# Kernel optimization log

Measured on AMD Instinct MI355X. Metric: run time of the kernel, lower is better.

## Reference

```python
import jax, jax.numpy as jnp
import numpy as np

NE, NPROC, E, D = 50000, 25000, 200000, 128
L, T = 3, 4  # layers, edge types: 0:e->e, 1:e->p, 2:p->p, 3:p->e


def setup_inputs() -> dict:
    key = jax.random.key(0)
    ks = jax.random.split(key, 17)
    s = 1.0 / np.sqrt(D)
    return {
        'x_elem': jax.random.normal(ks[0], (NE, D), jnp.float32),
        'x_proc': jax.random.normal(ks[1], (NPROC, D), jnp.float32),
        'W_src': jax.random.normal(ks[2], (L, T, D, D), jnp.float32) * s,
        'W_dst': jax.random.normal(ks[3], (L, T, D, D), jnp.float32) * s,
        'att_src': jax.random.normal(ks[4], (L, T, D), jnp.float32) * s,
        'att_dst': jax.random.normal(ks[5], (L, T, D), jnp.float32) * s,
        'bias': jax.random.normal(ks[6], (L, T, D), jnp.float32) * 0.01,
        'lin_W': jax.random.normal(ks[7], (D, 2), jnp.float32) * s,
        'lin_b': jnp.zeros((2,), jnp.float32),
        'ee_src': jax.random.randint(ks[8], (E,), 0, NE),
        'ee_dst': jax.random.randint(ks[9], (E,), 0, NE),
        'ep_src': jax.random.randint(ks[10], (E,), 0, NE),
        'ep_dst': jax.random.randint(ks[11], (E,), 0, NPROC),
        'pp_src': jax.random.randint(ks[12], (E,), 0, NPROC),
        'pp_dst': jax.random.randint(ks[13], (E,), 0, NPROC),
        'pe_src': jax.random.randint(ks[14], (E,), 0, NPROC),
        'pe_dst': jax.random.randint(ks[15], (E,), 0, NE),
    }


def _gat(x_s, x_d, src, dst, n_dst, Ws, Wd, a_s, a_d, b):
    # one GATConv (heads=1, negative_slope=0 -> relu, no self loops)
    hs = x_s @ Ws                       # [Ns, D]
    hd = x_d @ Wd                       # [Nd, D]
    es = hs @ a_s                       # [Ns]
    ed = hd @ a_d                       # [Nd]
    logit = jax.nn.relu(es[src] + ed[dst])              # [E]
    m = jax.ops.segment_max(logit, dst, num_segments=n_dst)
    m = jnp.where(jnp.isfinite(m), m, 0.0)              # empty segments
    w = jnp.exp(logit - m[dst])
    denom = jax.ops.segment_sum(w, dst, num_segments=n_dst)
    alpha = w / jnp.maximum(denom[dst], 1e-16)          # edge softmax per dst
    out = jax.ops.segment_sum(alpha[:, None] * hs[src], dst, num_segments=n_dst)
    return out + b


def reference(x_elem, x_proc, W_src, W_dst, att_src, att_dst, bias, lin_W, lin_b,
              ee_src, ee_dst, ep_src, ep_dst, pp_src, pp_dst, pe_src, pe_dst):
    xe, xp = x_elem, x_proc
    for l in range(L):
        ee = _gat(xe, xe, ee_src, ee_dst, NE, W_src[l, 0], W_dst[l, 0], att_src[l, 0], att_dst[l, 0], bias[l, 0])
        ep = _gat(xe, xp, ep_src, ep_dst, NPROC, W_src[l, 1], W_dst[l, 1], att_src[l, 1], att_dst[l, 1], bias[l, 1])
        pp = _gat(xp, xp, pp_src, pp_dst, NPROC, W_src[l, 2], W_dst[l, 2], att_src[l, 2], att_dst[l, 2], bias[l, 2])
        pe = _gat(xp, xe, pe_src, pe_dst, NE, W_src[l, 3], W_dst[l, 3], att_src[l, 3], att_dst[l, 3], bias[l, 3])
        xe = ee + pe   # to_hetero aggr='sum' per destination node type
        xp = ep + pp
    x = jnp.concatenate([xe, xp], axis=0) @ lin_W + lin_b  # G_aggr
    return x.mean(axis=0)  # [2]
```

## Files before the change

kernel.cpp:

```cpp
#include <hip/hip_runtime.h>

#define NE_N 50000
#define NP_N 25000
#define E_N 200000
#define DIM 128
#define LOG2E 1.4426950408889634f
#define NREP 1024

#define NCHK 32
#define CHK_E (E_N / NCHK)
#define TBL 16384

typedef __attribute__((ext_vector_type(8))) short short8;
typedef __attribute__((ext_vector_type(4))) float f32x4;
typedef __attribute__((ext_vector_type(2))) float f32x2;

static __device__ __forceinline__ ushort f2bf(float f) {
  unsigned x = __float_as_uint(f);
  return (ushort)((x + 0x7fffu + ((x >> 16) & 1u)) >> 16);
}
static __device__ __forceinline__ float bf2f(ushort u) {
  return __uint_as_float(((unsigned)u) << 16);
}

static __device__ __forceinline__ void gload_lds16(const void* g, void* l) {
  __builtin_amdgcn_global_load_lds(
      (const __attribute__((address_space(1))) void*)g,
      (__attribute__((address_space(3))) void*)l, 16, 0, 0);
}

#define HIST_BLKS (4 * NCHK)
#define HS_TOT (HIST_BLKS + 12 + 3)
__global__ __launch_bounds__(512) void hist_setup_k(
    const float* __restrict__ W_src, const float* __restrict__ W_dst,
    const float* __restrict__ att_dst, ushort* __restrict__ WbT,
    float* __restrict__ vec, const int* __restrict__ d0,
    const int* __restrict__ d1, const int* __restrict__ d2,
    const int* __restrict__ d3, unsigned char* __restrict__ h0,
    unsigned char* __restrict__ h1, unsigned char* __restrict__ h2,
    unsigned char* __restrict__ h3, ushort* __restrict__ rk0,
    ushort* __restrict__ rk1, ushort* __restrict__ rk2,
    ushort* __restrict__ rk3) {
  __shared__ int keys[TBL];
  __shared__ int cnts[TBL];
  const int blk = blockIdx.x;
  const int tid = threadIdx.x;
  if (blk < HIST_BLKS) {
    const int ty = blk >> 5, c = blk & (NCHK - 1);
    const int NN = (ty == 0 || ty == 3) ? NE_N : NP_N;
    const int* dst = ty == 0 ? d0 : ty == 1 ? d1 : ty == 2 ? d2 : d3;
    unsigned char* h = ty == 0 ? h0 : ty == 1 ? h1 : ty == 2 ? h2 : h3;
    ushort* rk = ty == 0 ? rk0 : ty == 1 ? rk1 : ty == 2 ? rk2 : rk3;
    for (int i = tid; i < TBL; i += 512) { keys[i] = -1; cnts[i] = 0; }
    __syncthreads();
    const int base = c * CHK_E;
    for (int i = tid; i < CHK_E; i += 512) {
      const int e = base + i;
      const int d = dst[e];
      unsigned hsh = ((unsigned)d * 2654435761u) >> 18;
      hsh &= (TBL - 1);
      int lr;
      while (true) {
        int prev = atomicCAS(&keys[hsh], -1, d);
        if (prev == -1 || prev == d) { lr = atomicAdd(&cnts[hsh], 1); break; }
        hsh = (hsh + 1) & (TBL - 1);
      }
      rk[e] = (ushort)lr;
    }
    __syncthreads();
    for (int i = tid; i < TBL; i += 512) {
      int k = keys[i];
      if (k >= 0) h[(size_t)c * NN + k] = (unsigned char)cnts[i];
    }
  } else if (blk < HIST_BLKS + 12) {
    const int w = blk - HIST_BLKS;
    const float* src = W_src + (size_t)w * DIM * DIM;
    ushort* dstw = WbT + (size_t)w * DIM * DIM;
    for (int i = tid; i < DIM * DIM; i += 512) {
      int k = i >> 7, n = i & 127;
      dstw[n * DIM + k] = f2bf(src[i]);
    }
  } else {
    const int b = blk - HIST_BLKS - 12;
    const int lt = b * 4 + (tid >> 7);
    const int i = tid & 127;
    const float* Wd = W_dst + (size_t)lt * DIM * DIM;
    const float* ad = att_dst + lt * DIM;
    float s = 0.f;
#pragma unroll 8
    for (int j = 0; j < DIM; j++) s += Wd[i * DIM + j] * ad[j];
    vec[lt * DIM + i] = s;
  }
}

__global__ __launch_bounds__(256) void scanA_k(
    unsigned char* __restrict__ h0, unsigned char* __restrict__ h1,
    unsigned char* __restrict__ h2, unsigned char* __restrict__ h3,
    int* __restrict__ c0, int* __restrict__ c1, int* __restrict__ c2,
    int* __restrict__ c3, int* __restrict__ part) {
  int ty = blockIdx.y;
  unsigned char* h = ty == 0 ? h0 : ty == 1 ? h1 : ty == 2 ? h2 : h3;
  int* cnt = ty == 0 ? c0 : ty == 1 ? c1 : ty == 2 ? c2 : c3;
  int n = (ty == 0 || ty == 3) ? NE_N : NP_N;
  int nblk = (n + 1023) >> 10;
  if ((int)blockIdx.x >= nblk) return;
  int base = blockIdx.x * 1024 + threadIdx.x * 4;
  int s = 0;
  if (base < n) {
    int run0 = 0, run1 = 0, run2 = 0, run3 = 0;
#pragma unroll
    for (int c = 0; c < NCHK; c++) {
      unsigned* hp = (unsigned*)(h + (size_t)c * n + base);
      unsigned v = *hp;
      *hp = (unsigned)(run0 & 255) | ((unsigned)(run1 & 255) << 8) |
            ((unsigned)(run2 & 255) << 16) | ((unsigned)(run3 & 255) << 24);
      run0 += (int)(v & 255u);
      run1 += (int)((v >> 8) & 255u);
      run2 += (int)((v >> 16) & 255u);
      run3 += (int)((v >> 24) & 255u);
    }
    cnt[base + 0] = run0; cnt[base + 1] = run1;
    cnt[base + 2] = run2; cnt[base + 3] = run3;
    s = run0 + run1 + run2 + run3;
  }
  int lane = threadIdx.x & 63, wid = threadIdx.x >> 6;
#pragma unroll
  for (int off = 32; off > 0; off >>= 1) s += __shfl_xor(s, off, 64);
  __shared__ int ws4[4];
  if (lane == 0) ws4[wid] = s;
  __syncthreads();
  if (threadIdx.x == 0)
    part[ty * 64 + blockIdx.x] = ws4[0] + ws4[1] + ws4[2] + ws4[3];
}

__global__ __launch_bounds__(256) void scanBC_k(
    const int* __restrict__ c0, const int* __restrict__ c1,
    const int* __restrict__ c2, const int* __restrict__ c3,
    int* __restrict__ r0, int* __restrict__ r1, int* __restrict__ r2,
    int* __restrict__ r3, const int* __restrict__ part) {
  int ty = blockIdx.y;
  int bx = blockIdx.x;
  const int* cnt = ty == 0 ? c0 : ty == 1 ? c1 : ty == 2 ? c2 : c3;
  int* rp = ty == 0 ? r0 : ty == 1 ? r1 : ty == 2 ? r2 : r3;
  int n = (ty == 0 || ty == 3) ? NE_N : NP_N;
  int nblk = (n + 1023) >> 10;
  if (bx >= nblk) return;

  __shared__ int s_excl;
  if (threadIdx.x < 64) {
    int pl = threadIdx.x;
    int v = (pl < nblk) ? part[ty * 64 + pl] : 0;
    int sc = v;
#pragma unroll
    for (int off = 1; off < 64; off <<= 1) {
      int t = __shfl_up(sc, off, 64);
      if (pl >= off) sc += t;
    }
    if (pl == bx) s_excl = sc - v;
  }
  if (bx == 0 && threadIdx.x == 0) rp[n] = E_N;
  __syncthreads();

  int base = bx * 1024 + threadIdx.x * 4;
  int v[4];
#pragma unroll
  for (int j = 0; j < 4; j++) v[j] = (base + j < n) ? cnt[base + j] : 0;
  int s = v[0] + v[1] + v[2] + v[3];
  int lane = threadIdx.x & 63, wid = threadIdx.x >> 6;
  int sc = s;
#pragma unroll
  for (int off = 1; off < 64; off <<= 1) {
    int t = __shfl_up(sc, off, 64);
    if (lane >= off) sc += t;
  }
  __shared__ int ws4[4];
  if (lane == 63) ws4[wid] = sc;
  __syncthreads();
  int wbase = 0;
  for (int w = 0; w < wid; w++) wbase += ws4[w];
  int p = s_excl + wbase + sc - s;
#pragma unroll
  for (int j = 0; j < 4; j++) {
    if (base + j < n) rp[base + j] = p;
    p += v[j];
  }
}

#define EBLK ((NE_N + 255) / 256)
#define PBLK ((NP_N + 255) / 256)
#define GEMM_BLK (EBLK + PBLK)
#define FILL_PER_CHK 13
#define FILL_BLKS (4 * NCHK * FILL_PER_CHK)
#define HG2_TOT (GEMM_BLK + FILL_BLKS)

template <bool FP32>
static __device__ __forceinline__ void x_prefetch(
    const void* xb, int rowA, int quad, float4* xraw, short8* xvv) {
  if (FP32) {
    const float* xf32 = (const float*)xb + (size_t)rowA * DIM + quad * 8;
#pragma unroll
    for (int k0 = 0; k0 < 4; k0++) {
      xraw[2 * k0] = *(const float4*)(xf32 + k0 * 32);
      xraw[2 * k0 + 1] = *(const float4*)(xf32 + k0 * 32 + 4);
    }
  } else {
    const ushort* xb16 = (const ushort*)xb + (size_t)rowA * DIM + quad * 8;
#pragma unroll
    for (int k0 = 0; k0 < 4; k0++)
      xvv[k0] = *(const short8*)(xb16 + k0 * 32);
  }
}

template <bool FP32>
static __device__ __forceinline__ void strip_body(
    int row0, int N, int m, int quad, int lane, const short8* wlds,
    const float* dv0, const float* dv1, const float* a0, const float* a1,
    unsigned char* hs0, unsigned char* hs1, float* es0, float* es1,
    float* edA, float* edB, float4* xraw, short8* xvv) {
  float edp0 = 0.f, edp1 = 0.f;
#pragma unroll
  for (int k0 = 0; k0 < 4; k0++) {
    float xf[8];
    if (FP32) {
      float4 f0 = xraw[2 * k0], f1 = xraw[2 * k0 + 1];
      xf[0] = f0.x; xf[1] = f0.y; xf[2] = f0.z; xf[3] = f0.w;
      xf[4] = f1.x; xf[5] = f1.y; xf[6] = f1.z; xf[7] = f1.w;
      short8 xv;
#pragma unroll
      for (int j = 0; j < 8; j++) xv[j] = (short)f2bf(xf[j]);
      xvv[k0] = xv;
    } else {
#pragma unroll
      for (int j = 0; j < 8; j++) xf[j] = bf2f((ushort)xvv[k0][j]);
    }
    int off = k0 * 32 + quad * 8;
    float4 vA0 = *(const float4*)&dv0[off];
    float4 vA1 = *(const float4*)&dv0[off + 4];
    float4 vB0 = *(const float4*)&dv1[off];
    float4 vB1 = *(const float4*)&dv1[off + 4];
    edp0 += xf[0] * vA0.x + xf[1] * vA0.y + xf[2] * vA0.z + xf[3] * vA0.w +
            xf[4] * vA1.x + xf[5] * vA1.y + xf[6] * vA1.z + xf[7] * vA1.w;
    edp1 += xf[0] * vB0.x + xf[1] * vB0.y + xf[2] * vB0.z + xf[3] * vB0.w +
            xf[4] * vB1.x + xf[5] * vB1.y + xf[6] * vB1.z + xf[7] * vB1.w;
  }

  f32x4 acc0[8], acc1[8];
#pragma unroll
  for (int f = 0; f < 8; f++) {
    acc0[f] = (f32x4){0.f, 0.f, 0.f, 0.f};
    acc1[f] = (f32x4){0.f, 0.f, 0.f, 0.f};
  }
#pragma unroll
  for (int k0 = 0; k0 < 4; k0++) {
    const short8 xv = xvv[k0];
#pragma unroll
    for (int f = 0; f < 8; f++) {
      acc0[f] = __builtin_amdgcn_mfma_f32_16x16x32_bf16(
          wlds[(k0 * 8 + f) * 64 + lane], xv, acc0[f], 0, 0, 0);
      acc1[f] = __builtin_amdgcn_mfma_f32_16x16x32_bf16(
          wlds[2048 + (k0 * 8 + f) * 64 + lane], xv, acc1[f], 0, 0, 0);
    }
  }

  const int row = row0 + m;
  edp0 += __shfl_xor(edp0, 16, 64);
  edp0 += __shfl_xor(edp0, 32, 64);
  edp1 += __shfl_xor(edp1, 16, 64);
  edp1 += __shfl_xor(edp1, 32, 64);
  if (quad == 0 && row < N) {
    edA[row] = edp0 * LOG2E;
    edB[row] = edp1 * LOG2E;
  }

#pragma unroll
  for (int set = 0; set < 2; set++) {
    f32x4* acc = set ? acc1 : acc0;
    const float* as = set ? a1 : a0;
    float* es = set ? es1 : es0;
    unsigned char* hs = set ? hs1 : hs0;

    float esum = 0.f;
#pragma unroll
    for (int f = 0; f < 8; f++) {
      float4 av = *(const float4*)&as[f * 16 + quad * 4];
      esum += acc[f][0] * av.x + acc[f][1] * av.y + acc[f][2] * av.z +
              acc[f][3] * av.w;
    }
    esum += __shfl_xor(esum, 16, 64);
    esum += __shfl_xor(esum, 32, 64);
    if (quad == 0 && row < N) es[row] = esum * LOG2E;

    if (row < N) {
#pragma unroll
      for (int f = 0; f < 8; f++) {
        int w = __builtin_amdgcn_cvt_pk_fp8_f32(acc[f][0], acc[f][1], 0, false);
        w = __builtin_amdgcn_cvt_pk_fp8_f32(acc[f][2], acc[f][3], w, true);
        *(unsigned*)&hs[(size_t)row * DIM + f * 16 + quad * 4] = (unsigned)w;
      }
    }
  }
}

template <bool FP32>
static __device__ __forceinline__ void gemm_body(
    int blk, const void* __restrict__ xev, const void* __restrict__ xpv,
    const ushort* __restrict__ WbT, const float* __restrict__ att,
    const float* __restrict__ vec, int l, unsigned char* __restrict__ hsE0,
    unsigned char* __restrict__ hsE1, unsigned char* __restrict__ hsP3,
    unsigned char* __restrict__ hsP2, float* __restrict__ esE0,
    float* __restrict__ esE1, float* __restrict__ esP3,
    float* __restrict__ esP2, float* __restrict__ edEA,
    float* __restrict__ edEB, float* __restrict__ edPA,
    float* __restrict__ edPB) {
  const void* xb;
  const ushort *W0T, *W1T;
  const float *a0, *a1, *dv0, *dv1;
  unsigned char *hs0, *hs1;
  float *es0, *es1, *edA, *edB;
  int N, rbase;
  if (blk < EBLK) {
    xb = xev; N = NE_N; rbase = blk * 256;
    W0T = WbT + (size_t)(l * 4 + 0) * DIM * DIM;
    W1T = WbT + (size_t)(l * 4 + 1) * DIM * DIM;
    a0 = att + (l * 4 + 0) * DIM; a1 = att + (l * 4 + 1) * DIM;
    dv0 = vec + (l * 4 + 0) * DIM; dv1 = vec + (l * 4 + 3) * DIM;
    hs0 = hsE0; hs1 = hsE1; es0 = esE0; es1 = esE1;
    edA = edEA; edB = edEB;
  } else {
    blk -= EBLK; xb = xpv; N = NP_N; rbase = blk * 256;
    W0T = WbT + (size_t)(l * 4 + 3) * DIM * DIM;
    W1T = WbT + (size_t)(l * 4 + 2) * DIM * DIM;
    a0 = att + (l * 4 + 3) * DIM; a1 = att + (l * 4 + 2) * DIM;
    dv0 = vec + (l * 4 + 1) * DIM; dv1 = vec + (l * 4 + 2) * DIM;
    hs0 = hsP3; hs1 = hsP2; es0 = esP3; es1 = esP2;
    edA = edPA; edB = edPB;
  }

  const int wave = threadIdx.x >> 6;
  const int lane = threadIdx.x & 63;
  const int m = lane & 15, quad = lane >> 4;
  const int row0A = rbase + wave * 16;
  const int row0B = rbase + 128 + wave * 16;
  int rowLA = row0A + m; if (rowLA >= N) rowLA = N - 1;
  int rowLB = row0B + m; if (rowLB >= N) rowLB = N - 1;

  float4 xrawA[8]; short8 xvvA[4];
  x_prefetch<FP32>(xb, rowLA, quad, xrawA, xvvA);

  __shared__ short8 wlds[4096];
  {
    const int i15 = lane & 15, i4 = lane >> 4;
#pragma unroll
    for (int r = 0; r < 8; r++) {
      const int g = r * 8 + wave;
      const int set = g >> 5, k0 = (g >> 3) & 3, f = g & 7;
      const ushort* WT = set ? W1T : W0T;
      gload_lds16(WT + (size_t)(f * 16 + i15) * DIM + k0 * 32 + i4 * 8,
                  &wlds[g * 64]);
    }
  }
  __syncthreads();

  float4 xrawB[8]; short8 xvvB[4];
  if (!FP32) x_prefetch<FP32>(xb, rowLB, quad, xrawB, xvvB);

  if (row0A < N)
    strip_body<FP32>(row0A, N, m, quad, lane, wlds, dv0, dv1, a0, a1,
                     hs0, hs1, es0, es1, edA, edB, xrawA, xvvA);
  if (FP32) x_prefetch<FP32>(xb, rowLB, quad, xrawB, xvvB);
  if (row0B < N)
    strip_body<FP32>(row0B, N, m, quad, lane, wlds, dv0, dv1, a0, a1,
                     hs0, hs1, es0, es1, edA, edB, xrawB, xvvB);
}

__global__ __launch_bounds__(512, 4) void gemm_k(
    const ushort* __restrict__ xe, const ushort* __restrict__ xp,
    const ushort* __restrict__ WbT, const float* __restrict__ att,
    const float* __restrict__ vec, int l, unsigned char* __restrict__ hsE0,
    unsigned char* __restrict__ hsE1, unsigned char* __restrict__ hsP3,
    unsigned char* __restrict__ hsP2, float* __restrict__ esE0,
    float* __restrict__ esE1, float* __restrict__ esP3,
    float* __restrict__ esP2, float* __restrict__ edEA,
    float* __restrict__ edEB, float* __restrict__ edPA,
    float* __restrict__ edPB) {
  gemm_body<false>(blockIdx.x, xe, xp, WbT, att, vec, l, hsE0, hsE1, hsP3,
                   hsP2, esE0, esE1, esP3, esP2, edEA, edEB, edPA, edPB);
}

__global__ __launch_bounds__(512, 4) void fill_gemm0_k(
    const float* __restrict__ xe, const float* __restrict__ xp,
    const ushort* __restrict__ WbT, const float* __restrict__ att,
    const float* __restrict__ vec, unsigned char* __restrict__ hsE0,
    unsigned char* __restrict__ hsE1, unsigned char* __restrict__ hsP3,
    unsigned char* __restrict__ hsP2, float* __restrict__ esE0,
    float* __restrict__ esE1, float* __restrict__ esP3,
    float* __restrict__ esP2, float* __restrict__ edEA,
    float* __restrict__ edEB, float* __restrict__ edPA,
    float* __restrict__ edPB, const int* __restrict__ s0,
    const int* __restrict__ s1, const int* __restrict__ s2,
    const int* __restrict__ s3, const int* __restrict__ d0,
    const int* __restrict__ d1, const int* __restrict__ d2,
    const int* __restrict__ d3, const ushort* __restrict__ rk0,
    const ushort* __restrict__ rk1, const ushort* __restrict__ rk2,
    const ushort* __restrict__ rk3, const int* __restrict__ r0,
    const int* __restrict__ r1, const int* __restrict__ r2,
    const int* __restrict__ r3, const unsigned char* __restrict__ h0,
    const unsigned char* __restrict__ h1, const unsigned char* __restrict__ h2,
    const unsigned char* __restrict__ h3, ushort* __restrict__ o0,
    ushort* __restrict__ o1, ushort* __restrict__ o2,
    ushort* __restrict__ o3) {
  const int blk = blockIdx.x;
  if (blk < GEMM_BLK) {
    gemm_body<true>(blk, xe, xp, WbT, att, vec, 0, hsE0, hsE1, hsP3, hsP2,
                    esE0, esE1, esP3, esP2, edEA, edEB, edPA, edPB);
  } else {
    const int fb = blk - GEMM_BLK;
    const int x = fb & 7, q = fb >> 3;
    const int g = ((q & 15) << 3) | x;
    const int j = q >> 4;
    const int i = j * 512 + threadIdx.x;
    if (i >= CHK_E) return;
    const int ty = g >> 5, c = g & 31;
    const int e = c * CHK_E + i;
    const int NN = (ty == 0 || ty == 3) ? NE_N : NP_N;
    const int* src = ty == 0 ? s0 : ty == 1 ? s1 : ty == 2 ? s2 : s3;
    const int* dst = ty == 0 ? d0 : ty == 1 ? d1 : ty == 2 ? d2 : d3;
    const ushort* rk = ty == 0 ? rk0 : ty == 1 ? rk1 : ty == 2 ? rk2 : rk3;
    const int* rp = ty == 0 ? r0 : ty == 1 ? r1 : ty == 2 ? r2 : r3;
    const unsigned char* ho = ty == 0 ? h0 : ty == 1 ? h1 : ty == 2 ? h2 : h3;
    ushort* out = ty == 0 ? o0 : ty == 1 ? o1 : ty == 2 ? o2 : o3;
    const int dd = dst[e];
    out[rp[dd] + (int)ho[(size_t)c * NN + dd] + (int)rk[e]] =
        (ushort)src[e];
  }
}

__global__ __launch_bounds__(256) void gat_gather_all(
    const int* __restrict__ rp0, const ushort* __restrict__ ss0,
    const int* __restrict__ rp1, const ushort* __restrict__ ss1,
    const int* __restrict__ rp2, const ushort* __restrict__ ss2,
    const int* __restrict__ rp3, const ushort* __restrict__ ss3,
    const float* __restrict__ esE0, const unsigned char* __restrict__ hsE0,
    const float* __restrict__ esE1, const unsigned char* __restrict__ hsE1,
    const float* __restrict__ esP3, const unsigned char* __restrict__ hsP3,
    const float* __restrict__ esP2, const unsigned char* __restrict__ hsP2,
    const float* __restrict__ edEA, const float* __restrict__ edEB,
    const float* __restrict__ edPA, const float* __restrict__ edPB,
    const float* __restrict__ bias, int l, ushort* __restrict__ outxe,
    ushort* __restrict__ outxp, int to_csum, float* __restrict__ csum_rep) {
  __shared__ float bufx[4][8 * 65];
  __shared__ float bufy[4][8 * 65];
  const int wid = (blockIdx.x * 256 + threadIdx.x) >> 6;
  const int lane = threadIdx.x & 63;
  const int wv = threadIdx.x >> 6;
  const int slot = lane >> 3, sub = lane & 7;
  const int half = slot >> 2;
  const int hslot = slot & 3;
  const bool active = wid < NE_N + NP_N;

  float v0 = 0.f, v1 = 0.f;
  const float *b0 = bias, *b1 = bias;
  ushort* outb = outxe;
  int node = 0;

  if (active) {
    const int *rpA, *rpB;
    const ushort *ssA, *ssB;
    const float *esA, *esB;
    const unsigned char *hsA, *hsB;
    const float *edA, *edB;
    if (wid < NE_N) {
      node = wid;
      rpA = rp0; ssA = ss0; esA = esE0; hsA = hsE0;
      rpB = rp3; ssB = ss3; esB = esP3; hsB = hsP3;
      edA = edEA; edB = edEB;
      b0 = bias + (l * 4 + 0) * DIM; b1 = bias + (l * 4 + 3) * DIM;
      outb = outxe;
    } else {
      node = wid - NE_N;
      rpA = rp1; ssA = ss1; esA = esE1; hsA = hsE1;
      rpB = rp2; ssB = ss2; esB = esP2; hsB = hsP2;
      edA = edPA; edB = edPB;
      b0 = bias + (l * 4 + 1) * DIM; b1 = bias + (l * 4 + 2) * DIM;
      outb = outxp;
    }

    const int* rp = half ? rpB : rpA;
    const ushort* ss = half ? ssB : ssA;
    const float* es = half ? esB : esA;
    const unsigned char* hs = half ? hsB : hsA;
    const float edv = half ? edB[node] : edA[node];
    const int beg = rp[node], end = rp[node + 1];

    f32x2 acc2[8];
#pragma unroll
    for (int j = 0; j < 8; j++) acc2[j] = (f32x2){0.f, 0.f};
    float sw = 0.f;

    for (int e = beg + hslot; e < end; e += 4) {
      int s = ss[e];
      float w = exp2f(fmaxf(es[s] + edv, 0.f));
      sw += w;
      f32x2 w2 = {w, w};
      uint4 h = *(const uint4*)&hs[(size_t)s * DIM + sub * 16];
      acc2[0] += w2 * __builtin_amdgcn_cvt_pk_f32_fp8((int)h.x, false);
      acc2[1] += w2 * __builtin_amdgcn_cvt_pk_f32_fp8((int)h.x, true);
      acc2[2] += w2 * __builtin_amdgcn_cvt_pk_f32_fp8((int)h.y, false);
      acc2[3] += w2 * __builtin_amdgcn_cvt_pk_f32_fp8((int)h.y, true);
      acc2[4] += w2 * __builtin_amdgcn_cvt_pk_f32_fp8((int)h.z, false);
      acc2[5] += w2 * __builtin_amdgcn_cvt_pk_f32_fp8((int)h.z, true);
      acc2[6] += w2 * __builtin_amdgcn_cvt_pk_f32_fp8((int)h.w, false);
      acc2[7] += w2 * __builtin_amdgcn_cvt_pk_f32_fp8((int)h.w, true);
    }

    sw += __shfl_xor(sw, 8, 64);
    sw += __shfl_xor(sw, 16, 64);
    const float inv = 1.f / fmaxf(sw, 1e-16f);

#pragma unroll
    for (int j = 0; j < 8; j++) {
      bufx[wv][slot * 65 + sub * 8 + j] = acc2[j].x * inv;
      bufy[wv][slot * 65 + sub * 8 + j] = acc2[j].y * inv;
    }
    float vx = 0.f, vy = 0.f;
#pragma unroll
    for (int s2 = 0; s2 < 8; s2++) {
      vx += bufx[wv][s2 * 65 + sub * 8 + slot];
      vy += bufy[wv][s2 * 65 + sub * 8 + slot];
    }
    v0 = vx;
    v1 = vy;
  }

  const int d = sub * 16 + slot * 2;
  if (to_csum) {
    __shared__ float lsum[4][DIM];
    lsum[wv][d] = v0;
    lsum[wv][d + 1] = v1;
    __syncthreads();
    if (threadIdx.x < DIM) {
      float s = lsum[0][threadIdx.x] + lsum[1][threadIdx.x] +
                lsum[2][threadIdx.x] + lsum[3][threadIdx.x];
      float* rep = csum_rep + (size_t)(blockIdx.x & (NREP - 1)) * DIM;
      unsafeAtomicAdd(&rep[threadIdx.x], s);
    }
  } else if (active) {
    float2 bb0 = *(const float2*)&b0[d];
    float2 bb1 = *(const float2*)&b1[d];
    ushort2 o;
    o.x = f2bf(v0 + bb0.x + bb1.x);
    o.y = f2bf(v1 + bb0.y + bb1.y);
    *(ushort2*)&outb[(size_t)node * DIM + d] = o;
  }
}

__global__ __launch_bounds__(512) void final_proj(
    const float* __restrict__ csum_rep, const float* __restrict__ bias,
    const float* __restrict__ lin_W, const float* __restrict__ lin_b,
    float* __restrict__ out) {
  __shared__ float parts[4][DIM];
  __shared__ float col[DIM];
  const int k = threadIdx.x & 127;
  const int pt = threadIdx.x >> 7;
  float s = 0.f;
#pragma unroll 8
  for (int r = pt * (NREP / 4); r < (pt + 1) * (NREP / 4); r++)
    s += csum_rep[(size_t)r * DIM + k];
  parts[pt][k] = s;
  __syncthreads();
  if (threadIdx.x < DIM) {
    const float* bE0 = bias + (2 * 4 + 0) * DIM;
    const float* bE1 = bias + (2 * 4 + 3) * DIM;
    const float* bP0 = bias + (2 * 4 + 1) * DIM;
    const float* bP1 = bias + (2 * 4 + 2) * DIM;
    col[k] = parts[0][k] + parts[1][k] + parts[2][k] + parts[3][k] +
             (float)NE_N * (bE0[k] + bE1[k]) +
             (float)NP_N * (bP0[k] + bP1[k]);
  }
  __syncthreads();
  if (threadIdx.x < 2) {
    float acc = 0.f;
#pragma unroll 8
    for (int j = 0; j < DIM; j++) acc += col[j] * lin_W[j * 2 + threadIdx.x];
    out[threadIdx.x] = acc / (float)(NE_N + NP_N) + lin_b[threadIdx.x];
  }
}

extern "C" void kernel_launch(void* const* d_in, const int* in_sizes, int n_in,
                              void* d_out, int out_size, void* d_ws,
                              size_t ws_size, hipStream_t stream) {
  const float* x_elem  = (const float*)d_in[0];
  const float* x_proc  = (const float*)d_in[1];
  const float* W_src   = (const float*)d_in[2];
  const float* W_dst   = (const float*)d_in[3];
  const float* att_src = (const float*)d_in[4];
  const float* att_dst = (const float*)d_in[5];
  const float* bias    = (const float*)d_in[6];
  const float* lin_W   = (const float*)d_in[7];
  const float* lin_b   = (const float*)d_in[8];
  const int* esrc[4] = {(const int*)d_in[9],  (const int*)d_in[11],
                        (const int*)d_in[13], (const int*)d_in[15]};
  const int* edst[4] = {(const int*)d_in[10], (const int*)d_in[12],
                        (const int*)d_in[14], (const int*)d_in[16]};

  char* p = (char*)d_ws;
  ushort* xe_bf[2]; ushort* xp_bf[2];
  xe_bf[0] = (ushort*)p; p += (size_t)NE_N * DIM * 2;
  xe_bf[1] = (ushort*)p; p += (size_t)NE_N * DIM * 2;
  xp_bf[0] = (ushort*)p; p += (size_t)NP_N * DIM * 2;
  xp_bf[1] = (ushort*)p; p += (size_t)NP_N * DIM * 2;
  unsigned char* hsE0 = (unsigned char*)p; p += (size_t)NE_N * DIM;
  unsigned char* hsE1 = (unsigned char*)p; p += (size_t)NE_N * DIM;
  unsigned char* hsP3 = (unsigned char*)p; p += (size_t)NP_N * DIM;
  unsigned char* hsP2 = (unsigned char*)p; p += (size_t)NP_N * DIM;
  ushort* WbT = (ushort*)p; p += (size_t)12 * DIM * DIM * 2;
  float* esE0 = (float*)p; p += (size_t)NE_N * 4;
  float* esE1 = (float*)p; p += (size_t)NE_N * 4;
  float* esP3 = (float*)p; p += (size_t)NP_N * 4;
  float* esP2 = (float*)p; p += (size_t)NP_N * 4;
  float* edEA = (float*)p; p += (size_t)NE_N * 4;
  float* edEB = (float*)p; p += (size_t)NE_N * 4;
  float* edPA = (float*)p; p += (size_t)NP_N * 4;
  float* edPB = (float*)p; p += (size_t)NP_N * 4;
  float* vec = (float*)p; p += 12 * DIM * 4;
  int* parti = (int*)p; p += 4 * 64 * 4;
  float* csum_rep = (float*)p; p += (size_t)NREP * DIM * 4;
  unsigned char* hh[4];
  hh[0] = (unsigned char*)p; p += (size_t)NE_N * NCHK;
  hh[1] = (unsigned char*)p; p += (size_t)NP_N * NCHK;
  hh[2] = (unsigned char*)p; p += (size_t)NP_N * NCHK;
  hh[3] = (unsigned char*)p; p += (size_t)NE_N * NCHK;
  int* cnt[4];
  for (int t = 0; t < 4; t++) { cnt[t] = (int*)p; p += (NE_N + 4) * 4; }
  int* rp[4];
  for (int t = 0; t < 4; t++) { rp[t] = (int*)p; p += (NE_N + 4) * 4; }
  ushort* ssrc[4];
  for (int t = 0; t < 4; t++) { ssrc[t] = (ushort*)p; p += (size_t)E_N * 2; }
  ushort* rank[4];
  for (int t = 0; t < 4; t++) { rank[t] = (ushort*)p; p += (size_t)E_N * 2; }

  hipMemsetAsync(csum_rep, 0,
                 (size_t)NREP * DIM * 4 +
                     (size_t)(2 * NE_N + 2 * NP_N) * NCHK,
                 stream);

  hist_setup_k<<<HS_TOT, 512, 0, stream>>>(
      W_src, W_dst, att_dst, WbT, vec, edst[0], edst[1], edst[2], edst[3],
      hh[0], hh[1], hh[2], hh[3], rank[0], rank[1], rank[2], rank[3]);

  scanA_k<<<dim3(49, 4), 256, 0, stream>>>(hh[0], hh[1], hh[2], hh[3],
                                           cnt[0], cnt[1], cnt[2], cnt[3],
                                           parti);
  scanBC_k<<<dim3(49, 4), 256, 0, stream>>>(cnt[0], cnt[1], cnt[2], cnt[3],
                                            rp[0], rp[1], rp[2], rp[3], parti);

  fill_gemm0_k<<<HG2_TOT, 512, 0, stream>>>(
      x_elem, x_proc, WbT, att_src, vec, hsE0, hsE1, hsP3, hsP2, esE0, esE1,
      esP3, esP2, edEA, edEB, edPA, edPB, esrc[0], esrc[1], esrc[2], esrc[3],
      edst[0], edst[1], edst[2], edst[3], rank[0], rank[1], rank[2], rank[3],
      rp[0], rp[1], rp[2], rp[3], hh[0], hh[1], hh[2], hh[3],
      ssrc[0], ssrc[1], ssrc[2], ssrc[3]);

  int c = 0;
  for (int l = 0; l < 3; l++) {
    if (l > 0) {
      gemm_k<<<GEMM_BLK, 512, 0, stream>>>(
          xe_bf[c], xp_bf[c], WbT, att_src, vec, l, hsE0, hsE1, hsP3, hsP2,
          esE0, esE1, esP3, esP2, edEA, edEB, edPA, edPB);
    }
    int to_csum = (l == 2) ? 1 : 0;
    gat_gather_all<<<(NE_N + NP_N) / 4, 256, 0, stream>>>(
        rp[0], ssrc[0], rp[1], ssrc[1], rp[2], ssrc[2], rp[3], ssrc[3], esE0,
        hsE0, esE1, hsE1, esP3, hsP3, esP2, hsP2, edEA, edEB, edPA, edPB,
        bias, l, xe_bf[1 - c], xp_bf[1 - c], to_csum, csum_rep);
    c = 1 - c;
  }

  final_proj<<<1, 512, 0, stream>>>(csum_rep, bias, lin_W, lin_b,
                                    (float*)d_out);
}
```

Baseline: 374.7 us.

## Replace random CSR scatter with two-pass bucketed scatter via LDS staging

```diff
diff --git a/kernel.cpp b/kernel.cpp
--- a/kernel.cpp
+++ b/kernel.cpp
@@ -10,6 +10,8 @@
 #define NCHK 32
 #define CHK_E (E_N / NCHK)
 #define TBL 16384
+
+#define NBKT ((E_N + 511) / 512)
 
 typedef __attribute__((ext_vector_type(8))) short short8;
 typedef __attribute__((ext_vector_type(4))) float f32x4;
@@ -189,9 +191,6 @@
 #define EBLK ((NE_N + 255) / 256)
 #define PBLK ((NP_N + 255) / 256)
 #define GEMM_BLK (EBLK + PBLK)
-#define FILL_PER_CHK 13
-#define FILL_BLKS (4 * NCHK * FILL_PER_CHK)
-#define HG2_TOT (GEMM_BLK + FILL_BLKS)
 
 template <bool FP32>
 static __device__ __forceinline__ void x_prefetch(
@@ -387,7 +386,7 @@
                    hsP2, esE0, esE1, esP3, esP2, edEA, edEB, edPA, edPB);
 }
 
-__global__ __launch_bounds__(512, 4) void fill_gemm0_k(
+__global__ __launch_bounds__(512, 4) void pos_gemm0_k(
     const float* __restrict__ xe, const float* __restrict__ xp,
     const ushort* __restrict__ WbT, const float* __restrict__ att,
     const float* __restrict__ vec, unsigned char* __restrict__ hsE0,
@@ -396,9 +395,7 @@
     float* __restrict__ esE1, float* __restrict__ esP3,
     float* __restrict__ esP2, float* __restrict__ edEA,
     float* __restrict__ edEB, float* __restrict__ edPA,
-    float* __restrict__ edPB, const int* __restrict__ s0,
-    const int* __restrict__ s1, const int* __restrict__ s2,
-    const int* __restrict__ s3, const int* __restrict__ d0,
+    float* __restrict__ edPB, const int* __restrict__ d0,
     const int* __restrict__ d1, const int* __restrict__ d2,
     const int* __restrict__ d3, const ushort* __restrict__ rk0,
     const ushort* __restrict__ rk1, const ushort* __restrict__ rk2,
@@ -406,32 +403,117 @@
     const int* __restrict__ r1, const int* __restrict__ r2,
     const int* __restrict__ r3, const unsigned char* __restrict__ h0,
     const unsigned char* __restrict__ h1, const unsigned char* __restrict__ h2,
-    const unsigned char* __restrict__ h3, ushort* __restrict__ o0,
-    ushort* __restrict__ o1, ushort* __restrict__ o2,
-    ushort* __restrict__ o3) {
+    const unsigned char* __restrict__ h3, int* __restrict__ p0,
+    int* __restrict__ p1, int* __restrict__ p2, int* __restrict__ p3,
+    ushort* __restrict__ cnt2) {
   const int blk = blockIdx.x;
   if (blk < GEMM_BLK) {
     gemm_body<true>(blk, xe, xp, WbT, att, vec, 0, hsE0, hsE1, hsP3, hsP2,
                     esE0, esE1, esP3, esP2, edEA, edEB, edPA, edPB);
   } else {
-    const int fb = blk - GEMM_BLK;
-    const int x = fb & 7, q = fb >> 3;
-    const int g = ((q & 15) << 3) | x;
-    const int j = q >> 4;
-    const int i = j * 512 + threadIdx.x;
-    if (i >= CHK_E) return;
-    const int ty = g >> 5, c = g & 31;
-    const int e = c * CHK_E + i;
+    __shared__ unsigned hcnt[NBKT];
+    const int pb = blk - GEMM_BLK;
+    const int ty = pb >> 5, c = pb & 31;
     const int NN = (ty == 0 || ty == 3) ? NE_N : NP_N;
-    const int* src = ty == 0 ? s0 : ty == 1 ? s1 : ty == 2 ? s2 : s3;
     const int* dst = ty == 0 ? d0 : ty == 1 ? d1 : ty == 2 ? d2 : d3;
     const ushort* rk = ty == 0 ? rk0 : ty == 1 ? rk1 : ty == 2 ? rk2 : rk3;
     const int* rp = ty == 0 ? r0 : ty == 1 ? r1 : ty == 2 ? r2 : r3;
     const unsigned char* ho = ty == 0 ? h0 : ty == 1 ? h1 : ty == 2 ? h2 : h3;
-    ushort* out = ty == 0 ? o0 : ty == 1 ? o1 : ty == 2 ? o2 : o3;
-    const int dd = dst[e];
-    out[rp[dd] + (int)ho[(size_t)c * NN + dd] + (int)rk[e]] =
-        (ushort)src[e];
+    int* ps = ty == 0 ? p0 : ty == 1 ? p1 : ty == 2 ? p2 : p3;
+    ushort* c2 = cnt2 + (size_t)(ty * NCHK + c) * NBKT;
+    const int tid = threadIdx.x;
+    for (int i = tid; i < NBKT; i += 512) hcnt[i] = 0;
+    __syncthreads();
+    const int base = c * CHK_E;
+    for (int i = tid; i < CHK_E; i += 512) {
+      const int e = base + i;
+      const int dd = dst[e];
+      const int pos = rp[dd] + (int)ho[(size_t)c * NN + dd] + (int)rk[e];
+      ps[e] = pos;
+      atomicAdd(&hcnt[pos >> 9], 1u);
+    }
+    __syncthreads();
+    for (int i = tid; i < NBKT; i += 512) c2[i] = (ushort)hcnt[i];
+  }
+}
+
+__global__ __launch_bounds__(512) void f1_k(
+    const int* __restrict__ s0, const int* __restrict__ s1,
+    const int* __restrict__ s2, const int* __restrict__ s3,
+    const int* __restrict__ p0, const int* __restrict__ p1,
+    const int* __restrict__ p2, const int* __restrict__ p3,
+    const ushort* __restrict__ cnt2, unsigned* __restrict__ rec0,
+    unsigned* __restrict__ rec1, unsigned* __restrict__ rec2,
+    unsigned* __restrict__ rec3) {
+  const int ty = blockIdx.x >> 5, c = blockIdx.x & 31;
+  const int* src = ty == 0 ? s0 : ty == 1 ? s1 : ty == 2 ? s2 : s3;
+  const int* ps = ty == 0 ? p0 : ty == 1 ? p1 : ty == 2 ? p2 : p3;
+  const ushort* c2t = cnt2 + (size_t)ty * NCHK * NBKT;
+  unsigned* rec = ty == 0 ? rec0 : ty == 1 ? rec1 : ty == 2 ? rec2 : rec3;
+
+  __shared__ unsigned gOff[NBKT];
+  __shared__ unsigned lBase[NBKT];
+  __shared__ unsigned cur[NBKT];
+  __shared__ unsigned stag[CHK_E];
+  __shared__ unsigned wsum[8];
+  const int tid = threadIdx.x;
+  const int lane = tid & 63, wv = tid >> 6;
+
+  unsigned vown = 0;
+  if (tid < NBKT) {
+    vown = c2t[(size_t)c * NBKT + tid];
+    unsigned sp = 0;
+    for (int cc = 0; cc < c; cc++) sp += c2t[(size_t)cc * NBKT + tid];
+    gOff[tid] = ((unsigned)tid << 9) + sp;
+  }
+  unsigned sc = vown;
+#pragma unroll
+  for (int off = 1; off < 64; off <<= 1) {
+    unsigned t = __shfl_up(sc, off, 64);
+    if (lane >= off) sc += t;
+  }
+  if (lane == 63) wsum[wv] = sc;
+  __syncthreads();
+  unsigned wb = 0;
+  for (int w = 0; w < wv; w++) wb += wsum[w];
+  if (tid < NBKT) {
+    unsigned excl = wb + sc - vown;
+    lBase[tid] = excl;
+    cur[tid] = excl;
+  }
+  __syncthreads();
+
+  const int base = c * CHK_E;
+  for (int i = tid; i < CHK_E; i += 512) {
+    const int e = base + i;
+    const int pos = ps[e];
+    const int b = pos >> 9;
+    unsigned slot = atomicAdd(&cur[b], 1u);
+    stag[slot] = ((unsigned)src[e] << 9) | (unsigned)(pos & 511);
+  }
+  __syncthreads();
+
+  for (int b = wv; b < NBKT; b += 8) {
+    const unsigned lb = lBase[b];
+    const unsigned n = cur[b] - lb;
+    const unsigned g = gOff[b];
+    for (unsigned i = lane; i < n; i += 64) rec[g + i] = stag[lb + i];
+  }
+}
+
+__global__ __launch_bounds__(512) void f2_k(
+    const unsigned* __restrict__ rec0, const unsigned* __restrict__ rec1,
+    const unsigned* __restrict__ rec2, const unsigned* __restrict__ rec3,
+    ushort* __restrict__ o0, ushort* __restrict__ o1,
+    ushort* __restrict__ o2, ushort* __restrict__ o3) {
+  const int ty = blockIdx.x / NBKT, b = blockIdx.x % NBKT;
+  const unsigned* rec = ty == 0 ? rec0 : ty == 1 ? rec1 : ty == 2 ? rec2 : rec3;
+  ushort* out = ty == 0 ? o0 : ty == 1 ? o1 : ty == 2 ? o2 : o3;
+  const int base = b << 9;
+  const int n = min(512, E_N - base);
+  if ((int)threadIdx.x < n) {
+    const unsigned r = rec[base + threadIdx.x];
+    out[base + (int)(r & 511u)] = (ushort)(r >> 9);
   }
 }
 
@@ -638,6 +720,11 @@
   for (int t = 0; t < 4; t++) { ssrc[t] = (ushort*)p; p += (size_t)E_N * 2; }
   ushort* rank[4];
   for (int t = 0; t < 4; t++) { rank[t] = (ushort*)p; p += (size_t)E_N * 2; }
+  int* pos32[4];
+  for (int t = 0; t < 4; t++) { pos32[t] = (int*)p; p += (size_t)E_N * 4; }
+  unsigned* rec[4];
+  for (int t = 0; t < 4; t++) { rec[t] = (unsigned*)p; p += (size_t)E_N * 4; }
+  ushort* cnt2 = (ushort*)p; p += (size_t)4 * NCHK * NBKT * 2;
 
   hipMemsetAsync(csum_rep, 0,
                  (size_t)NREP * DIM * 4 +
@@ -654,12 +741,17 @@
   scanBC_k<<<dim3(49, 4), 256, 0, stream>>>(cnt[0], cnt[1], cnt[2], cnt[3],
                                             rp[0], rp[1], rp[2], rp[3], parti);
 
-  fill_gemm0_k<<<HG2_TOT, 512, 0, stream>>>(
+  pos_gemm0_k<<<GEMM_BLK + 4 * NCHK, 512, 0, stream>>>(
       x_elem, x_proc, WbT, att_src, vec, hsE0, hsE1, hsP3, hsP2, esE0, esE1,
-      esP3, esP2, edEA, edEB, edPA, edPB, esrc[0], esrc[1], esrc[2], esrc[3],
-      edst[0], edst[1], edst[2], edst[3], rank[0], rank[1], rank[2], rank[3],
-      rp[0], rp[1], rp[2], rp[3], hh[0], hh[1], hh[2], hh[3],
-      ssrc[0], ssrc[1], ssrc[2], ssrc[3]);
+      esP3, esP2, edEA, edEB, edPA, edPB, edst[0], edst[1], edst[2], edst[3],
+      rank[0], rank[1], rank[2], rank[3], rp[0], rp[1], rp[2], rp[3],
+      hh[0], hh[1], hh[2], hh[3], pos32[0], pos32[1], pos32[2], pos32[3],
+      cnt2);
+  f1_k<<<4 * NCHK, 512, 0, stream>>>(
+      esrc[0], esrc[1], esrc[2], esrc[3], pos32[0], pos32[1], pos32[2],
+      pos32[3], cnt2, rec[0], rec[1], rec[2], rec[3]);
+  f2_k<<<4 * NBKT, 512, 0, stream>>>(rec[0], rec[1], rec[2], rec[3],
+                                     ssrc[0], ssrc[1], ssrc[2], ssrc[3]);
 
   int c = 0;
   for (int l = 0; l < 3; l++) {
```

Result: slower. 394.8 us (+5.4%).

## Map one destination node per 16 lanes and reduce with shuffles instead of LDS

Applied to the files above, without the earlier changes.

```diff
diff --git a/kernel.cpp b/kernel.cpp
--- a/kernel.cpp
+++ b/kernel.cpp
@@ -448,95 +448,92 @@
     const float* __restrict__ edPA, const float* __restrict__ edPB,
     const float* __restrict__ bias, int l, ushort* __restrict__ outxe,
     ushort* __restrict__ outxp, int to_csum, float* __restrict__ csum_rep) {
-  __shared__ float bufx[4][8 * 65];
-  __shared__ float bufy[4][8 * 65];
-  const int wid = (blockIdx.x * 256 + threadIdx.x) >> 6;
   const int lane = threadIdx.x & 63;
   const int wv = threadIdx.x >> 6;
-  const int slot = lane >> 3, sub = lane & 7;
-  const int half = slot >> 2;
-  const int hslot = slot & 3;
+  const int half = (lane >> 3) & 1;
+  const int sub = lane & 7;
+  const int wid = (blockIdx.x * 256 + threadIdx.x) >> 4;
   const bool active = wid < NE_N + NP_N;
 
-  float v0 = 0.f, v1 = 0.f;
   const float *b0 = bias, *b1 = bias;
   ushort* outb = outxe;
   int node = 0;
+  int beg = 0, end = 0;
+  const ushort* ss = ss0;
+  const float* es = esE0;
+  const unsigned char* hs = hsE0;
+  float edv = 0.f;
 
   if (active) {
-    const int *rpA, *rpB;
-    const ushort *ssA, *ssB;
-    const float *esA, *esB;
-    const unsigned char *hsA, *hsB;
-    const float *edA, *edB;
     if (wid < NE_N) {
       node = wid;
-      rpA = rp0; ssA = ss0; esA = esE0; hsA = hsE0;
-      rpB = rp3; ssB = ss3; esB = esP3; hsB = hsP3;
-      edA = edEA; edB = edEB;
+      if (half == 0) { ss = ss0; es = esE0; hs = hsE0; edv = edEA[node];
+                       beg = rp0[node]; end = rp0[node + 1]; }
+      else           { ss = ss3; es = esP3; hs = hsP3; edv = edEB[node];
+                       beg = rp3[node]; end = rp3[node + 1]; }
       b0 = bias + (l * 4 + 0) * DIM; b1 = bias + (l * 4 + 3) * DIM;
       outb = outxe;
     } else {
       node = wid - NE_N;
-      rpA = rp1; ssA = ss1; esA = esE1; hsA = hsE1;
-      rpB = rp2; ssB = ss2; esB = esP2; hsB = hsP2;
-      edA = edPA; edB = edPB;
+      if (half == 0) { ss = ss1; es = esE1; hs = hsE1; edv = edPA[node];
+                       beg = rp1[node]; end = rp1[node + 1]; }
+      else           { ss = ss2; es = esP2; hs = hsP2; edv = edPB[node];
+                       beg = rp2[node]; end = rp2[node + 1]; }
       b0 = bias + (l * 4 + 1) * DIM; b1 = bias + (l * 4 + 2) * DIM;
       outb = outxp;
     }
-
-    const int* rp = half ? rpB : rpA;
-    const ushort* ss = half ? ssB : ssA;
-    const float* es = half ? esB : esA;
-    const unsigned char* hs = half ? hsB : hsA;
-    const float edv = half ? edB[node] : edA[node];
-    const int beg = rp[node], end = rp[node + 1];
-
-    f32x2 acc2[8];
-#pragma unroll
-    for (int j = 0; j < 8; j++) acc2[j] = (f32x2){0.f, 0.f};
-    float sw = 0.f;
-
-    for (int e = beg + hslot; e < end; e += 4) {
-      int s = ss[e];
-      float w = exp2f(fmaxf(es[s] + edv, 0.f));
-      sw += w;
-      f32x2 w2 = {w, w};
-      uint4 h = *(const uint4*)&hs[(size_t)s * DIM + sub * 16];
-      acc2[0] += w2 * __builtin_amdgcn_cvt_pk_f32_fp8((int)h.x, false);
-      acc2[1] += w2 * __builtin_amdgcn_cvt_pk_f32_fp8((int)h.x, true);
-      acc2[2] += w2 * __builtin_amdgcn_cvt_pk_f32_fp8((int)h.y, false);
-      acc2[3] += w2 * __builtin_amdgcn_cvt_pk_f32_fp8((int)h.y, true);
-      acc2[4] += w2 * __builtin_amdgcn_cvt_pk_f32_fp8((int)h.z, false);
-      acc2[5] += w2 * __builtin_amdgcn_cvt_pk_f32_fp8((int)h.z, true);
-      acc2[6] += w2 * __builtin_amdgcn_cvt_pk_f32_fp8((int)h.w, false);
-      acc2[7] += w2 * __builtin_amdgcn_cvt_pk_f32_fp8((int)h.w, true);
-    }
-
-    sw += __shfl_xor(sw, 8, 64);
-    sw += __shfl_xor(sw, 16, 64);
-    const float inv = 1.f / fmaxf(sw, 1e-16f);
-
+  }
+
+  f32x2 acc2[8];
+#pragma unroll
+  for (int j = 0; j < 8; j++) acc2[j] = (f32x2){0.f, 0.f};
+  float sw = 0.f;
+
+  for (int e = beg; e < end; e++) {
+    int s = ss[e];
+    float w = exp2f(fmaxf(es[s] + edv, 0.f));
+    sw += w;
+    f32x2 w2 = {w, w};
+    uint4 h = *(const uint4*)&hs[(size_t)s * DIM + sub * 16];
+    acc2[0] += w2 * __builtin_amdgcn_cvt_pk_f32_fp8((int)h.x, false);
+    acc2[1] += w2 * __builtin_amdgcn_cvt_pk_f32_fp8((int)h.x, true);
+    acc2[2] += w2 * __builtin_amdgcn_cvt_pk_f32_fp8((int)h.y, false);
+    acc2[3] += w2 * __builtin_amdgcn_cvt_pk_f32_fp8((int)h.y, true);
+    acc2[4] += w2 * __builtin_amdgcn_cvt_pk_f32_fp8((int)h.z, false);
+    acc2[5] += w2 * __builtin_amdgcn_cvt_pk_f32_fp8((int)h.z, true);
+    acc2[6] += w2 * __builtin_amdgcn_cvt_pk_f32_fp8((int)h.w, false);
+    acc2[7] += w2 * __builtin_amdgcn_cvt_pk_f32_fp8((int)h.w, true);
+  }
+
+  const float inv = 1.f / fmaxf(sw, 1e-16f);
+#pragma unroll
+  for (int j = 0; j < 8; j++) {
+    acc2[j].x *= inv;
+    acc2[j].y *= inv;
+    f32x2 t;
+    t.x = __shfl_xor(acc2[j].x, 8, 64);
+    t.y = __shfl_xor(acc2[j].y, 8, 64);
+    acc2[j] += t;
+  }
+
+  if (to_csum) {
 #pragma unroll
     for (int j = 0; j < 8; j++) {
-      bufx[wv][slot * 65 + sub * 8 + j] = acc2[j].x * inv;
-      bufy[wv][slot * 65 + sub * 8 + j] = acc2[j].y * inv;
-    }
-    float vx = 0.f, vy = 0.f;
-#pragma unroll
-    for (int s2 = 0; s2 < 8; s2++) {
-      vx += bufx[wv][s2 * 65 + sub * 8 + slot];
-      vy += bufy[wv][s2 * 65 + sub * 8 + slot];
-    }
-    v0 = vx;
-    v1 = vy;
-  }
-
-  const int d = sub * 16 + slot * 2;
-  if (to_csum) {
+      f32x2 t;
+      t.x = __shfl_xor(acc2[j].x, 16, 64);
+      t.y = __shfl_xor(acc2[j].y, 16, 64);
+      acc2[j] += t;
+      t.x = __shfl_xor(acc2[j].x, 32, 64);
+      t.y = __shfl_xor(acc2[j].y, 32, 64);
+      acc2[j] += t;
+    }
     __shared__ float lsum[4][DIM];
-    lsum[wv][d] = v0;
-    lsum[wv][d + 1] = v1;
+    if (lane < 8) {
+#pragma unroll
+      for (int j = 0; j < 8; j++)
+        *(float2*)&lsum[wv][sub * 16 + 2 * j] =
+            make_float2(acc2[j].x, acc2[j].y);
+    }
     __syncthreads();
     if (threadIdx.x < DIM) {
       float s = lsum[0][threadIdx.x] + lsum[1][threadIdx.x] +
@@ -544,13 +541,20 @@
       float* rep = csum_rep + (size_t)(blockIdx.x & (NREP - 1)) * DIM;
       unsafeAtomicAdd(&rep[threadIdx.x], s);
     }
-  } else if (active) {
-    float2 bb0 = *(const float2*)&b0[d];
-    float2 bb1 = *(const float2*)&b1[d];
-    ushort2 o;
-    o.x = f2bf(v0 + bb0.x + bb1.x);
-    o.y = f2bf(v1 + bb0.y + bb1.y);
-    *(ushort2*)&outb[(size_t)node * DIM + d] = o;
+  } else if (active && half == 0) {
+    unsigned ow[8];
+#pragma unroll
+    for (int j = 0; j < 8; j++) {
+      const int d = sub * 16 + 2 * j;
+      float2 bb0 = *(const float2*)&b0[d];
+      float2 bb1 = *(const float2*)&b1[d];
+      unsigned lo = f2bf(acc2[j].x + bb0.x + bb1.x);
+      unsigned hi = f2bf(acc2[j].y + bb0.y + bb1.y);
+      ow[j] = lo | (hi << 16);
+    }
+    uint4* op = (uint4*)&outb[(size_t)node * DIM + sub * 16];
+    op[0] = make_uint4(ow[0], ow[1], ow[2], ow[3]);
+    op[1] = make_uint4(ow[4], ow[5], ow[6], ow[7]);
   }
 }
 
@@ -669,7 +673,7 @@
           esE0, esE1, esP3, esP2, edEA, edEB, edPA, edPB);
     }
     int to_csum = (l == 2) ? 1 : 0;
-    gat_gather_all<<<(NE_N + NP_N) / 4, 256, 0, stream>>>(
+    gat_gather_all<<<(NE_N + NP_N + 15) / 16, 256, 0, stream>>>(
         rp[0], ssrc[0], rp[1], ssrc[1], rp[2], ssrc[2], rp[3], ssrc[3], esE0,
         hsE0, esE1, hsE1, esP3, hsP3, esP2, hsP2, edEA, edEB, edPA, edPB,
         bias, l, xe_bf[1 - c], xp_bf[1 - c], to_csum, csum_rep);
```

Result: faster. 359.5 us (-4.1%).
